# Performance work log

Hardware: AMD Instinct MI355X
Metric: run time of the kernel (lower is better)

The kernel has to match this reference:

```python
import jax, jax.numpy as jnp
import numpy as np
from jax import lax

EPS = 1e-5


def binarize(x):
    return jnp.sign(x)


def conv3x3(x, w):
    # x: NCHW, w: OIHW, stride 1, padding 1 (SAME for k=3)
    return lax.conv_general_dilated(
        x, w, window_strides=(1, 1), padding=((1, 1), (1, 1)),
        dimension_numbers=("NCHW", "OIHW", "NCHW"))


def prelu(x, a):
    # a broadcastable per-channel slope
    return jnp.where(x >= 0, x, a * x)


def bn(x, gamma, beta, axes):
    mean = jnp.mean(x, axis=axes, keepdims=True)
    var = jnp.var(x, axis=axes, keepdims=True)
    shp = [1] * x.ndim
    shp[1] = x.shape[1]
    g = gamma.reshape(shp)
    b = beta.reshape(shp)
    return (x - mean) * lax.rsqrt(var + EPS) * g + b


def setup_inputs() -> dict:
    key = jax.random.key(0)
    ks = jax.random.split(key, 8)
    B = 256
    C = [1, 64, 128]
    FC_IN = 28 * 28 * C[-1]  # 100352
    F1, F2 = 1024, 10
    inp = {
        "x": jax.random.normal(ks[0], (B, C[0], 28, 28), jnp.float32),
        "cw0": jax.random.normal(ks[1], (C[1], C[0], 3, 3), jnp.float32) * 0.1,
        "cp0": jnp.full((C[1],), 0.25, jnp.float32),
        "cg0": jnp.ones((C[1],), jnp.float32),
        "cb0": jnp.zeros((C[1],), jnp.float32),
        "cw1": jax.random.normal(ks[2], (C[2], C[1], 3, 3), jnp.float32) * 0.1,
        "cp1": jnp.full((C[2],), 0.25, jnp.float32),
        "cg1": jnp.ones((C[2],), jnp.float32),
        "cb1": jnp.zeros((C[2],), jnp.float32),
        "fw0": jax.random.normal(ks[3], (F1, FC_IN), jnp.float32) * 0.02,
        "fp0": jnp.full((F1,), 0.25, jnp.float32),
        "fg0": jnp.ones((F1,), jnp.float32),
        "fb0": jnp.zeros((F1,), jnp.float32),
        "fw1": jax.random.normal(ks[4], (F2, F1), jnp.float32) * 0.05,
        "fp1": jnp.full((F2,), 0.25, jnp.float32),
        "fg1": jnp.ones((F2,), jnp.float32),
        "fb1": jnp.zeros((F2,), jnp.float32),
        "scale": jnp.ones((1,), jnp.float32),
    }
    return inp


def reference(x, cw0, cp0, cg0, cb0, cw1, cp1, cg1, cb1,
              fw0, fp0, fg0, fb0, fw1, fp1, fg1, fb1, scale):
    # conv block 0
    h = binarize(x)
    h = conv3x3(h, jnp.sign(cw0))
    h = prelu(h, cp0[None, :, None, None])
    h = bn(h, cg0, cb0, axes=(0, 2, 3))
    # conv block 1
    h = binarize(h)
    h = conv3x3(h, jnp.sign(cw1))
    h = prelu(h, cp1[None, :, None, None])
    h = bn(h, cg1, cb1, axes=(0, 2, 3))
    # flatten
    h = h.reshape(-1, 28 * 28 * cw1.shape[0])
    # fc block 0
    h = binarize(h)
    h = h @ jnp.sign(fw0).T
    h = prelu(h, fp0[None, :])
    h = bn(h, fg0, fb0, axes=(0,))
    # fc block 1
    h = binarize(h)
    h = h @ jnp.sign(fw1).T
    h = prelu(h, fp1[None, :])
    h = bn(h, fg1, fb1, axes=(0,))
    # scale layer
    return h * scale
```

## Files before the change

### kernel.cpp

```cpp
#include <hip/hip_runtime.h>
#include <stdint.h>


static constexpr int BATCH = 256;
static constexpr int K0    = 100352;
static constexpr int KW    = 1568;
static constexpr int N1    = 1024;
static constexpr int KS2   = 49;
static constexpr int JW2   = 32;
static constexpr int SUB2  = 8;
static constexpr int NS2   = 4;
static constexpr unsigned ZCAP = 65536;

__device__ __forceinline__ float fsign(float v){
    return (v > 0.f) ? 1.f : ((v < 0.f) ? -1.f : 0.f);
}

__global__ __launch_bounds__(256) void k_pack_w1(const float* __restrict__ cw1,
        uint64_t* __restrict__ wn1, uint64_t* __restrict__ wnz1,
        int* __restrict__ zero_region)
{
    if (blockIdx.x == 0) {
        for (int i = threadIdx.x; i < 512; i += 256) zero_region[i] = 0;
    }
    int idx = blockIdx.x*4 + (threadIdx.x >> 6);
    int lane = threadIdx.x & 63;
    int oc = idx / 9, t = idx % 9;
    float w = cw1[oc*576 + lane*9 + t];
    uint64_t n = __ballot(w < 0.f);
    uint64_t z = __ballot(w != 0.f);
    if (lane == 0) { wn1[idx] = n; wnz1[idx] = z; }
}

__global__ __launch_bounds__(256) void k_conv0(const float* __restrict__ x,
        const float* __restrict__ cw0, const float* __restrict__ cp0,
        int8_t* __restrict__ h0s, double* __restrict__ S0, double* __restrict__ Q0)
{
    __shared__ float img[30][30];
    __shared__ float redS[4][64];
    __shared__ float redQ[4][64];
    int b = blockIdx.x;
    int tid = threadIdx.x;
    for (int i = tid; i < 900; i += 256) ((float*)img)[i] = 0.f;
    __syncthreads();
    for (int i = tid; i < 784; i += 256) {
        float v = x[b*784 + i];
        img[1 + i/28][1 + i%28] = fsign(v);
    }
    __syncthreads();
    int lane = tid & 63, wv = tid >> 6;
    float wsg[9];
    #pragma unroll
    for (int t = 0; t < 9; t++) wsg[t] = fsign(cw0[lane*9 + t]);
    float a = cp0[lane];
    float accS = 0.f, accQ = 0.f;
    for (int i = 0; i < 196; i++) {
        int p = wv*196 + i;
        int y = p / 28, xx = p % 28;
        float s = 0.f;
        #pragma unroll
        for (int dy = 0; dy < 3; dy++)
            #pragma unroll
            for (int dx = 0; dx < 3; dx++)
                s += img[y+dy][xx+dx] * wsg[dy*3+dx];
        h0s[(size_t)(b*784 + p)*64 + lane] = (int8_t)(int)s;
        float v = (s >= 0.f) ? s : a*s;
        accS += v; accQ += v*v;
    }
    redS[wv][lane] = accS; redQ[wv][lane] = accQ;
    __syncthreads();
    if (tid < 64) {
        double s = (double)redS[0][tid] + redS[1][tid] + redS[2][tid] + redS[3][tid];
        double q = (double)redQ[0][tid] + redQ[1][tid] + redQ[2][tid] + redQ[3][tid];
        atomicAdd(&S0[tid], s);
        atomicAdd(&Q0[tid], q);
    }
}

__global__ __launch_bounds__(256) void k_pack_h0(const int8_t* __restrict__ h0s,
        const double* __restrict__ S0, const double* __restrict__ Q0,
        const float* __restrict__ cg0, const float* __restrict__ cb0,
        const float* __restrict__ cp0, uint64_t* __restrict__ hp)
{
    __shared__ unsigned l[64];
    int tid = threadIdx.x;
    if (tid < 64) {
        double mean = S0[tid] * (1.0/200704.0);
        double var  = Q0[tid] * (1.0/200704.0) - mean*mean;
        if (var < 0.0) var = 0.0;
        double A = (double)cg0[tid] / sqrt(var + 1e-5);
        double B = (double)cb0[tid] - mean*A;
        float a = cp0[tid];
        unsigned m = 0;
        for (int s = -9; s <= 9; ++s) {
            float v = (s >= 0) ? (float)s : a*(float)s;
            if (fma((double)v, A, B) < 0.0) m |= 1u << (s + 9);
        }
        l[tid] = m;
    }
    __syncthreads();
    int pixel = blockIdx.x*256 + tid;
    const int4* p4 = (const int4*)(h0s + (size_t)pixel*64);
    int4 va = p4[0], vb = p4[1], vc = p4[2], vd = p4[3];
    int wa[16] = {va.x,va.y,va.z,va.w, vb.x,vb.y,vb.z,vb.w,
                  vc.x,vc.y,vc.z,vc.w, vd.x,vd.y,vd.z,vd.w};
    unsigned lo = 0, hi = 0;
    #pragma unroll
    for (int wi = 0; wi < 16; ++wi) {
        unsigned w = (unsigned)wa[wi];
        #pragma unroll
        for (int c2 = 0; c2 < 4; ++c2) {
            int ch = wi*4 + c2;
            int s = (int)(signed char)(w >> (8*c2));
            unsigned bit = (l[ch] >> (s + 9)) & 1u;
            if (ch < 32) lo |= bit << ch; else hi |= bit << (ch - 32);
        }
    }
    hp[pixel] = ((uint64_t)hi << 32) | lo;
}

__global__ __launch_bounds__(256) void k_conv1(const uint64_t* __restrict__ hp,
        const uint64_t* __restrict__ wn1, const uint64_t* __restrict__ wnz1,
        const float* __restrict__ cp1, int16_t* __restrict__ h1s,
        double* __restrict__ pS1, double* __restrict__ pQ1)
{
    __shared__ float lS[4][8];
    __shared__ float lQ[4][8];
    int bid = blockIdx.x;
    int ocg = bid & 15;
    int ptg = (bid >> 4) & 3;
    int b   = bid >> 6;
    int wv = threadIdx.x >> 6, lane = threadIdx.x & 63;
    int pt = ptg*4 + wv;
    bool active = (pt < 13);
    int p = active ? (pt*64 + lane) : 0;
    bool pvalid = active && (p < 784);
    int y = p / 28, xx = p % 28;
    uint64_t nb[9]; unsigned vmask = 0;
    #pragma unroll
    for (int dy = 0; dy < 3; dy++)
        #pragma unroll
        for (int dx = 0; dx < 3; dx++) {
            int t = dy*3+dx;
            int yy = y + dy - 1, xv = xx + dx - 1;
            bool ok = (yy >= 0 && yy < 28 && xv >= 0 && xv < 28);
            nb[t] = hp[b*784 + (ok ? (yy*28+xv) : 0)];
            if (ok) vmask |= 1u << t;
        }
    #pragma unroll
    for (int o = 0; o < 8; o++) {
        int oc = ocg*8 + o;
        int base = oc*9;
        int acc = 0;
        #pragma unroll
        for (int t = 0; t < 9; t++) {
            uint64_t wn = wn1[base+t], wz = wnz1[base+t];
            if (vmask & (1u<<t))
                acc += (int)__popcll(wz) - 2*(int)__popcll((nb[t] ^ wn) & wz);
        }
        if (pvalid) h1s[((size_t)b*128 + oc)*784 + p] = (int16_t)acc;
        float pr = cp1[oc];
        float v = pvalid ? ((acc >= 0) ? (float)acc : pr*(float)acc) : 0.f;
        float s = v, q = v*v;
        #pragma unroll
        for (int off = 32; off; off >>= 1) {
            s += __shfl_xor(s, off);
            q += __shfl_xor(q, off);
        }
        if (lane == 0) { lS[wv][o] = s; lQ[wv][o] = q; }
    }
    __syncthreads();
    if (threadIdx.x < 16) {
        int o = threadIdx.x & 7;
        bool isQ = threadIdx.x >= 8;
        double v4 = isQ ? ((double)lQ[0][o] + lQ[1][o] + lQ[2][o] + lQ[3][o])
                        : ((double)lS[0][o] + lS[1][o] + lS[2][o] + lS[3][o]);
        double* dst = isQ ? pQ1 : pS1;
        dst[(size_t)(ocg*8 + o)*1024 + (b*4 + ptg)] = v4;
    }
}

__global__ __launch_bounds__(256) void k_bnfin1(const double* __restrict__ pS,
        const double* __restrict__ pQ, const float* __restrict__ g,
        const float* __restrict__ bb, double* __restrict__ AB)
{
    int oc = blockIdx.x;
    int tid = threadIdx.x;
    double s = 0.0, q = 0.0;
    #pragma unroll
    for (int i = 0; i < 4; ++i) {
        s += pS[(size_t)oc*1024 + tid + 256*i];
        q += pQ[(size_t)oc*1024 + tid + 256*i];
    }
    __shared__ double rs[256], rq[256];
    rs[tid] = s; rq[tid] = q;
    __syncthreads();
    for (int off = 128; off; off >>= 1) {
        if (tid < off) { rs[tid] += rs[tid+off]; rq[tid] += rq[tid+off]; }
        __syncthreads();
    }
    if (tid == 0) {
        double mean = rs[0] * (1.0/200704.0);
        double var  = rq[0] * (1.0/200704.0) - mean*mean;
        if (var < 0.0) var = 0.0;
        double A = (double)g[oc] / sqrt(var + 1e-5);
        AB[oc] = A; AB[128 + oc] = (double)bb[oc] - mean*A;
    }
}

__global__ __launch_bounds__(256) void k_pack_a0(const int16_t* __restrict__ h1s,
        const float* __restrict__ cp1, const double* __restrict__ AB,
        uint64_t* __restrict__ ap_t)
{
    int blk = blockIdx.x;
    int b  = blk / 98;
    int qg = blk % 98;
    int wv = threadIdx.x >> 6, lane = threadIdx.x & 63;
    int q  = qg*4 + wv;
    int k0 = q*256 + lane*4;
    short4 sv = *(const short4*)(h1s + (size_t)b*K0 + k0);
    int oc = k0 / 784;
    double A = AB[oc], B = AB[128 + oc];
    float a = cp1[oc];
    int ss[4] = {sv.x, sv.y, sv.z, sv.w};
    uint64_t words[4];
    #pragma unroll
    for (int c = 0; c < 4; ++c) {
        float s = (float)ss[c];
        float v = (s >= 0.f) ? s : a*s;
        double t = fma((double)v, A, B);
        words[c] = __ballot(t < 0.0);
    }
    if (lane == 0) {
        #pragma unroll
        for (int c = 0; c < 4; ++c)
            ap_t[(size_t)(4*q + c)*256 + b] = words[c];
    }
}

__global__ __launch_bounds__(256) void k_fc0g(const float* __restrict__ fw0,
        const uint64_t* __restrict__ ap_t, int16_t* __restrict__ pcpart,
        unsigned* __restrict__ zcnt, uint64_t* __restrict__ zlist)
{
    __shared__ uint64_t wT[32][33];
    __shared__ uint64_t apL[SUB2][256];
    int ks = blockIdx.x % KS2;
    int nt = blockIdx.x / KS2;
    int tid = threadIdx.x;
    int wv = tid >> 6, lane = tid & 63;
    int n0 = nt*32, j0 = ks*JW2;
    {
        const float* wsrc = fw0 + (size_t)(n0 + wv*8)*K0 + (size_t)(ks*8)*256 + lane*4;
        for (int r8 = 0; r8 < 8; ++r8) {
            const float* rowp = wsrc + (size_t)r8*K0;
            int row = wv*8 + r8;
            #pragma unroll
            for (int qq = 0; qq < 8; ++qq) {
                float4 w = *(const float4*)(rowp + qq*256);
                uint64_t g0 = __ballot(w.x < 0.f);
                uint64_t g1 = __ballot(w.y < 0.f);
                uint64_t g2 = __ballot(w.z < 0.f);
                uint64_t g3 = __ballot(w.w < 0.f);
                uint64_t z0 = __ballot(w.x == 0.f);
                uint64_t z1 = __ballot(w.y == 0.f);
                uint64_t z2 = __ballot(w.z == 0.f);
                uint64_t z3 = __ballot(w.w == 0.f);
                if (lane == 0) {
                    wT[row][qq*4+0] = g0;
                    wT[row][qq*4+1] = g1;
                    wT[row][qq*4+2] = g2;
                    wT[row][qq*4+3] = g3;
                    uint64_t zz[4] = {z0, z1, z2, z3};
                    #pragma unroll
                    for (int c = 0; c < 4; ++c) if (zz[c]) {
                        unsigned id = atomicAdd(zcnt, 1u);
                        if (id < ZCAP) {
                            unsigned j = (unsigned)((ks*8 + qq)*4 + c);
                            zlist[2*id]   = ((uint64_t)(unsigned)(n0+row) << 32) | j;
                            zlist[2*id+1] = zz[c];
                        }
                    }
                }
            }
        }
    }
    int bq = tid & 31;
    int nq = tid >> 5;
    int pc[8][4];
    #pragma unroll
    for (int i = 0; i < 8; i++)
        #pragma unroll
        for (int k = 0; k < 4; k++) pc[i][k] = 0;
    for (int c = 0; c < NS2; c++) {
        #pragma unroll
        for (int r = 0; r < SUB2; r++)
            apL[r][tid] = ap_t[(size_t)(j0 + c*SUB2 + r)*256 + tid];
        __syncthreads();
        #pragma unroll
        for (int jj = 0; jj < SUB2; jj++) {
            uint64_t aw[8], ww[4];
            #pragma unroll
            for (int i = 0; i < 8; i++) aw[i] = apL[jj][bq + 32*i];
            #pragma unroll
            for (int k = 0; k < 4; k++) ww[k] = wT[nq + 8*k][c*8 + jj];
            #pragma unroll
            for (int i = 0; i < 8; i++)
                #pragma unroll
                for (int k = 0; k < 4; k++)
                    pc[i][k] += (int)__popcll(aw[i] ^ ww[k]);
        }
        __syncthreads();
    }
    #pragma unroll
    for (int k = 0; k < 4; k++) {
        int n = n0 + nq + 8*k;
        #pragma unroll
        for (int i = 0; i < 8; i++)
            pcpart[((size_t)ks*N1 + n)*BATCH + (bq + 32*i)] = (int16_t)pc[i][k];
    }
}

__global__ __launch_bounds__(256) void k_fc0ep(const int16_t* __restrict__ pcpart,
        const unsigned* __restrict__ zcnt, const uint64_t* __restrict__ zlist,
        const uint64_t* __restrict__ ap_t, const float* __restrict__ fp0,
        const float* __restrict__ fg0, const float* __restrict__ fb0,
        float* __restrict__ af)
{
    int n = blockIdx.x, b = threadIdx.x;
    int pc = 0;
    #pragma unroll
    for (int ks = 0; ks < KS2; ks++) pc += (int)pcpart[((size_t)ks*N1 + n)*BATCH + b];
    int s = K0 - 2*pc;
    unsigned cnt = *zcnt; if (cnt > ZCAP) cnt = ZCAP;
    for (unsigned e = 0; e < cnt; ++e) {
        uint64_t key = zlist[2*e];
        if ((int)(key >> 32) == n) {
            uint64_t zm = zlist[2*e+1];
            uint64_t a = ap_t[(size_t)(key & 0xffffffffu)*256 + b];
            s += 2*(int)__popcll(a & zm) - (int)__popcll(zm);
        }
    }
    float a = fp0[n];
    float v = (s >= 0) ? (float)s : a*(float)s;
    __shared__ double rs[256], rq[256];
    rs[b] = v; rq[b] = (double)v*(double)v;
    __syncthreads();
    for (int off=128; off>0; off>>=1){
        if (b<off){ rs[b]+=rs[b+off]; rq[b]+=rq[b+off]; }
        __syncthreads();
    }
    __shared__ double AB[2];
    if (b == 0) {
        double mean = rs[0] / 256.0;
        double var = rq[0] / 256.0 - mean*mean;
        if (var < 0.0) var = 0.0;
        double A = (double)fg0[n] / sqrt(var + 1e-5);
        AB[0] = A; AB[1] = (double)fb0[n] - mean*A;
    }
    __syncthreads();
    double t = fma((double)v, AB[0], AB[1]);
    af[(size_t)n*256 + b] = (t > 0.0) ? 1.f : ((t < 0.0) ? -1.f : 0.f);
}

__global__ __launch_bounds__(256) void k_fc1a(const float* __restrict__ af,
        const float* __restrict__ fw1, float* __restrict__ part9)
{
    __shared__ float swL[10][32];
    int ks = blockIdx.x, b = threadIdx.x;
    for (int i = b; i < 320; i += 256) {
        int j = i / 32, kk = i % 32;
        swL[j][kk] = fsign(fw1[j*1024 + ks*32 + kk]);
    }
    __syncthreads();
    float acc[10];
    #pragma unroll
    for (int j=0;j<10;j++) acc[j]=0.f;
    for (int kk = 0; kk < 32; kk++) {
        float a = af[(size_t)(ks*32+kk)*256 + b];
        #pragma unroll
        for (int j=0;j<10;j++) acc[j] += a * swL[j][kk];
    }
    #pragma unroll
    for (int j=0;j<10;j++) part9[((size_t)ks*256 + b)*10 + j] = acc[j];
}

__global__ __launch_bounds__(256) void k_fc1b(const float* __restrict__ part9,
        const float* __restrict__ fp1, const float* __restrict__ fg1,
        const float* __restrict__ fb1, const float* __restrict__ scale,
        float* __restrict__ out)
{
    int b = threadIdx.x;
    float v[10];
    #pragma unroll
    for (int j=0;j<10;j++) v[j]=0.f;
    for (int ks=0; ks<32; ks++)
        #pragma unroll
        for (int j=0;j<10;j++) v[j] += part9[((size_t)ks*256+b)*10 + j];
    #pragma unroll
    for (int j=0;j<10;j++){
        float a = fp1[j];
        v[j] = (v[j] >= 0.f) ? v[j] : a*v[j];
    }
    __shared__ double sv[256];
    __shared__ double AB[2][10];
    for (int j=0;j<10;j++){
        sv[b] = (double)v[j];
        __syncthreads();
        for (int off=128;off>0;off>>=1){ if(b<off) sv[b]+=sv[b+off]; __syncthreads(); }
        double mean = sv[0]/256.0;
        __syncthreads();
        double d = (double)v[j]-mean;
        sv[b] = d*d;
        __syncthreads();
        for (int off=128;off>0;off>>=1){ if(b<off) sv[b]+=sv[b+off]; __syncthreads(); }
        if (b==0){
            double var = sv[0]/256.0;
            double A = (double)fg1[j]/sqrt(var+1e-5);
            AB[0][j]=A; AB[1][j]=(double)fb1[j] - mean*A;
        }
        __syncthreads();
    }
    float sc = scale[0];
    #pragma unroll
    for (int j=0;j<10;j++)
        out[b*10+j] = (float)fma((double)v[j], AB[0][j], AB[1][j]) * sc;
}

extern "C" void kernel_launch(void* const* d_in, const int* in_sizes, int n_in,
                              void* d_out, int out_size, void* d_ws, size_t ws_size,
                              hipStream_t stream)
{
    const float* x    = (const float*)d_in[0];
    const float* cw0  = (const float*)d_in[1];
    const float* cp0  = (const float*)d_in[2];
    const float* cg0  = (const float*)d_in[3];
    const float* cb0  = (const float*)d_in[4];
    const float* cw1  = (const float*)d_in[5];
    const float* cp1  = (const float*)d_in[6];
    const float* cg1  = (const float*)d_in[7];
    const float* cb1  = (const float*)d_in[8];
    const float* fw0  = (const float*)d_in[9];
    const float* fp0  = (const float*)d_in[10];
    const float* fg0  = (const float*)d_in[11];
    const float* fb0  = (const float*)d_in[12];
    const float* fw1  = (const float*)d_in[13];
    const float* fp1  = (const float*)d_in[14];
    const float* fg1  = (const float*)d_in[15];
    const float* fb1  = (const float*)d_in[16];
    const float* scale= (const float*)d_in[17];

    char* ws = (char*)d_ws;
    size_t off = 0;
    auto alloc = [&](size_t bytes)->char* {
        char* r = ws + off; off = (off + bytes + 255) & ~(size_t)255; return r; };

    double*   S0    = (double*)alloc(64*8);
    double*   Q0    = (double*)alloc(64*8);
    unsigned* zcnt  = (unsigned*)alloc(256);
    double*   A1B1  = (double*)alloc(256*8);
    double*   pS1   = (double*)alloc((size_t)128*1024*8);
    double*   pQ1   = (double*)alloc((size_t)128*1024*8);
    int8_t*   h0s   = (int8_t*)alloc((size_t)256*784*64);
    uint64_t* hp    = (uint64_t*)alloc((size_t)256*784*8);
    int16_t*  h1s   = (int16_t*)alloc((size_t)256*128*784*2);
    uint64_t* ap_t  = (uint64_t*)alloc((size_t)KW*256*8);
    uint64_t* wn1   = (uint64_t*)alloc(1152*8);
    uint64_t* wnz1  = (uint64_t*)alloc(1152*8);
    int16_t*  pcpart= (int16_t*)alloc((size_t)KS2*N1*BATCH*2);
    float*    af    = (float*)alloc((size_t)1024*256*4);
    float*    part9 = (float*)alloc((size_t)32*256*10*4);
    uint64_t* zlist = (uint64_t*)alloc((size_t)ZCAP*16);
    (void)ws_size; (void)in_sizes; (void)n_in; (void)out_size;

    k_pack_w1<<<288,     256, 0, stream>>>(cw1, wn1, wnz1, (int*)d_ws);
    k_conv0  <<<256,     256, 0, stream>>>(x, cw0, cp0, h0s, S0, Q0);
    k_pack_h0<<<784,     256, 0, stream>>>(h0s, S0, Q0, cg0, cb0, cp0, hp);
    k_conv1  <<<16384,   256, 0, stream>>>(hp, wn1, wnz1, cp1, h1s, pS1, pQ1);
    k_bnfin1 <<<128,     256, 0, stream>>>(pS1, pQ1, cg1, cb1, A1B1);
    k_pack_a0<<<256*98,  256, 0, stream>>>(h1s, cp1, A1B1, ap_t);
    k_fc0g   <<<KS2*32,  256, 0, stream>>>(fw0, ap_t, pcpart, zcnt, zlist);
    k_fc0ep  <<<1024,    256, 0, stream>>>(pcpart, zcnt, zlist, ap_t, fp0, fg0, fb0, af);
    k_fc1a   <<<32,      256, 0, stream>>>(af, fw1, part9);
    k_fc1b   <<<1,       256, 0, stream>>>(part9, fp1, fg1, fb1, scale, (float*)d_out);
}
```

Baseline: 350.6 us.

## Loop conv1 over pixel groups per block, precompute weight popcounts, fuse fc1 kernels

```diff
diff --git a/kernel.cpp b/kernel.cpp
--- a/kernel.cpp
+++ b/kernel.cpp
@@ -18,10 +18,10 @@
 
 __global__ __launch_bounds__(256) void k_pack_w1(const float* __restrict__ cw1,
         uint64_t* __restrict__ wn1, uint64_t* __restrict__ wnz1,
-        int* __restrict__ zero_region)
+        int* __restrict__ wzc, int* __restrict__ zero_region)
 {
     if (blockIdx.x == 0) {
-        for (int i = threadIdx.x; i < 512; i += 256) zero_region[i] = 0;
+        for (int i = threadIdx.x; i < 320; i += 256) zero_region[i] = 0;
     }
     int idx = blockIdx.x*4 + (threadIdx.x >> 6);
     int lane = threadIdx.x & 63;
@@ -29,7 +29,7 @@
     float w = cw1[oc*576 + lane*9 + t];
     uint64_t n = __ballot(w < 0.f);
     uint64_t z = __ballot(w != 0.f);
-    if (lane == 0) { wn1[idx] = n; wnz1[idx] = z; }
+    if (lane == 0) { wn1[idx] = n; wnz1[idx] = z; wzc[idx] = (int)__popcll(z); }
 }
 
 __global__ __launch_bounds__(256) void k_conv0(const float* __restrict__ x,
@@ -121,47 +121,58 @@
 
 __global__ __launch_bounds__(256) void k_conv1(const uint64_t* __restrict__ hp,
         const uint64_t* __restrict__ wn1, const uint64_t* __restrict__ wnz1,
-        const float* __restrict__ cp1, int16_t* __restrict__ h1s,
-        double* __restrict__ pS1, double* __restrict__ pQ1)
+        const int* __restrict__ wzc, const float* __restrict__ cp1,
+        int16_t* __restrict__ h1s, double* __restrict__ pS1, double* __restrict__ pQ1)
 {
     __shared__ float lS[4][8];
     __shared__ float lQ[4][8];
     int bid = blockIdx.x;
     int ocg = bid & 15;
-    int ptg = (bid >> 4) & 3;
-    int b   = bid >> 6;
+    int b   = bid >> 4;
     int wv = threadIdx.x >> 6, lane = threadIdx.x & 63;
-    int pt = ptg*4 + wv;
-    bool active = (pt < 13);
-    int p = active ? (pt*64 + lane) : 0;
-    bool pvalid = active && (p < 784);
-    int y = p / 28, xx = p % 28;
-    uint64_t nb[9]; unsigned vmask = 0;
-    #pragma unroll
-    for (int dy = 0; dy < 3; dy++)
-        #pragma unroll
-        for (int dx = 0; dx < 3; dx++) {
-            int t = dy*3+dx;
-            int yy = y + dy - 1, xv = xx + dx - 1;
-            bool ok = (yy >= 0 && yy < 28 && xv >= 0 && xv < 28);
-            nb[t] = hp[b*784 + (ok ? (yy*28+xv) : 0)];
-            if (ok) vmask |= 1u << t;
-        }
+    float pr[8];
+    #pragma unroll
+    for (int o = 0; o < 8; o++) pr[o] = cp1[ocg*8 + o];
+    float sA[8], qA[8];
+    #pragma unroll
+    for (int o = 0; o < 8; o++) { sA[o] = 0.f; qA[o] = 0.f; }
+
+    for (int ptg = 0; ptg < 4; ++ptg) {
+        int pt = ptg*4 + wv;
+        bool active = (pt < 13);
+        int p = active ? (pt*64 + lane) : 0;
+        bool pvalid = active && (p < 784);
+        int y = p / 28, xx = p % 28;
+        uint64_t nb[9]; unsigned vmask = 0;
+        #pragma unroll
+        for (int dy = 0; dy < 3; dy++)
+            #pragma unroll
+            for (int dx = 0; dx < 3; dx++) {
+                int t = dy*3+dx;
+                int yy = y + dy - 1, xv = xx + dx - 1;
+                bool ok = (yy >= 0 && yy < 28 && xv >= 0 && xv < 28);
+                nb[t] = hp[b*784 + (ok ? (yy*28+xv) : 0)];
+                if (ok) vmask |= 1u << t;
+            }
+        #pragma unroll
+        for (int o = 0; o < 8; o++) {
+            int base = (ocg*8 + o)*9;
+            int acc = 0;
+            #pragma unroll
+            for (int t = 0; t < 9; t++) {
+                uint64_t wn = wn1[base+t], wz = wnz1[base+t];
+                int wc = wzc[base+t];
+                if (vmask & (1u<<t))
+                    acc += wc - 2*(int)__popcll((nb[t] ^ wn) & wz);
+            }
+            if (pvalid) h1s[((size_t)b*128 + ocg*8 + o)*784 + p] = (int16_t)acc;
+            float v = pvalid ? ((acc >= 0) ? (float)acc : pr[o]*(float)acc) : 0.f;
+            sA[o] += v; qA[o] += v*v;
+        }
+    }
     #pragma unroll
     for (int o = 0; o < 8; o++) {
-        int oc = ocg*8 + o;
-        int base = oc*9;
-        int acc = 0;
-        #pragma unroll
-        for (int t = 0; t < 9; t++) {
-            uint64_t wn = wn1[base+t], wz = wnz1[base+t];
-            if (vmask & (1u<<t))
-                acc += (int)__popcll(wz) - 2*(int)__popcll((nb[t] ^ wn) & wz);
-        }
-        if (pvalid) h1s[((size_t)b*128 + oc)*784 + p] = (int16_t)acc;
-        float pr = cp1[oc];
-        float v = pvalid ? ((acc >= 0) ? (float)acc : pr*(float)acc) : 0.f;
-        float s = v, q = v*v;
+        float s = sA[o], q = qA[o];
         #pragma unroll
         for (int off = 32; off; off >>= 1) {
             s += __shfl_xor(s, off);
@@ -176,7 +187,7 @@
         double v4 = isQ ? ((double)lQ[0][o] + lQ[1][o] + lQ[2][o] + lQ[3][o])
                         : ((double)lS[0][o] + lS[1][o] + lS[2][o] + lS[3][o]);
         double* dst = isQ ? pQ1 : pS1;
-        dst[(size_t)(ocg*8 + o)*1024 + (b*4 + ptg)] = v4;
+        dst[(size_t)(ocg*8 + o)*256 + b] = v4;
     }
 }
 
@@ -186,14 +197,9 @@
 {
     int oc = blockIdx.x;
     int tid = threadIdx.x;
-    double s = 0.0, q = 0.0;
-    #pragma unroll
-    for (int i = 0; i < 4; ++i) {
-        s += pS[(size_t)oc*1024 + tid + 256*i];
-        q += pQ[(size_t)oc*1024 + tid + 256*i];
-    }
     __shared__ double rs[256], rq[256];
-    rs[tid] = s; rq[tid] = q;
+    rs[tid] = pS[(size_t)oc*256 + tid];
+    rq[tid] = pQ[(size_t)oc*256 + tid];
     __syncthreads();
     for (int off = 128; off; off >>= 1) {
         if (tid < off) { rs[tid] += rs[tid+off]; rq[tid] += rq[tid+off]; }
@@ -270,14 +276,16 @@
                     wT[row][qq*4+1] = g1;
                     wT[row][qq*4+2] = g2;
                     wT[row][qq*4+3] = g3;
-                    uint64_t zz[4] = {z0, z1, z2, z3};
-                    #pragma unroll
-                    for (int c = 0; c < 4; ++c) if (zz[c]) {
-                        unsigned id = atomicAdd(zcnt, 1u);
-                        if (id < ZCAP) {
-                            unsigned j = (unsigned)((ks*8 + qq)*4 + c);
-                            zlist[2*id]   = ((uint64_t)(unsigned)(n0+row) << 32) | j;
-                            zlist[2*id+1] = zz[c];
+                    if (z0 | z1 | z2 | z3) {
+                        uint64_t zz[4] = {z0, z1, z2, z3};
+                        #pragma unroll
+                        for (int c = 0; c < 4; ++c) if (zz[c]) {
+                            unsigned id = atomicAdd(zcnt, 1u);
+                            if (id < ZCAP) {
+                                unsigned j = (unsigned)((ks*8 + qq)*4 + c);
+                                zlist[2*id]   = ((uint64_t)(unsigned)(n0+row) << 32) | j;
+                                zlist[2*id+1] = zz[c];
+                            }
                         }
                     }
                 }
@@ -362,68 +370,41 @@
     af[(size_t)n*256 + b] = (t > 0.0) ? 1.f : ((t < 0.0) ? -1.f : 0.f);
 }
 
-__global__ __launch_bounds__(256) void k_fc1a(const float* __restrict__ af,
-        const float* __restrict__ fw1, float* __restrict__ part9)
-{
-    __shared__ float swL[10][32];
-    int ks = blockIdx.x, b = threadIdx.x;
-    for (int i = b; i < 320; i += 256) {
-        int j = i / 32, kk = i % 32;
-        swL[j][kk] = fsign(fw1[j*1024 + ks*32 + kk]);
-    }
-    __syncthreads();
-    float acc[10];
-    #pragma unroll
-    for (int j=0;j<10;j++) acc[j]=0.f;
-    for (int kk = 0; kk < 32; kk++) {
-        float a = af[(size_t)(ks*32+kk)*256 + b];
-        #pragma unroll
-        for (int j=0;j<10;j++) acc[j] += a * swL[j][kk];
-    }
-    #pragma unroll
-    for (int j=0;j<10;j++) part9[((size_t)ks*256 + b)*10 + j] = acc[j];
-}
-
-__global__ __launch_bounds__(256) void k_fc1b(const float* __restrict__ part9,
-        const float* __restrict__ fp1, const float* __restrict__ fg1,
-        const float* __restrict__ fb1, const float* __restrict__ scale,
-        float* __restrict__ out)
-{
-    int b = threadIdx.x;
-    float v[10];
-    #pragma unroll
-    for (int j=0;j<10;j++) v[j]=0.f;
-    for (int ks=0; ks<32; ks++)
-        #pragma unroll
-        for (int j=0;j<10;j++) v[j] += part9[((size_t)ks*256+b)*10 + j];
-    #pragma unroll
-    for (int j=0;j<10;j++){
-        float a = fp1[j];
-        v[j] = (v[j] >= 0.f) ? v[j] : a*v[j];
-    }
+__global__ __launch_bounds__(256) void k_fc1(const float* __restrict__ af,
+        const float* __restrict__ fw1, const float* __restrict__ fp1,
+        const float* __restrict__ fg1, const float* __restrict__ fb1,
+        const float* __restrict__ scale, float* __restrict__ out)
+{
     __shared__ double sv[256];
-    __shared__ double AB[2][10];
-    for (int j=0;j<10;j++){
-        sv[b] = (double)v[j];
-        __syncthreads();
-        for (int off=128;off>0;off>>=1){ if(b<off) sv[b]+=sv[b+off]; __syncthreads(); }
-        double mean = sv[0]/256.0;
-        __syncthreads();
-        double d = (double)v[j]-mean;
-        sv[b] = d*d;
-        __syncthreads();
-        for (int off=128;off>0;off>>=1){ if(b<off) sv[b]+=sv[b+off]; __syncthreads(); }
-        if (b==0){
-            double var = sv[0]/256.0;
-            double A = (double)fg1[j]/sqrt(var+1e-5);
-            AB[0][j]=A; AB[1][j]=(double)fb1[j] - mean*A;
-        }
-        __syncthreads();
-    }
-    float sc = scale[0];
-    #pragma unroll
-    for (int j=0;j<10;j++)
-        out[b*10+j] = (float)fma((double)v[j], AB[0][j], AB[1][j]) * sc;
+    __shared__ double ABj[2];
+    int j = blockIdx.x, b = threadIdx.x;
+    float acc = 0.f;
+    for (int k = 0; k < 1024; ++k)
+        acc += af[(size_t)k*256 + b] * fsign(fw1[j*1024 + k]);
+    float a = fp1[j];
+    float v = (acc >= 0.f) ? acc : a*acc;
+    sv[b] = (double)v;
+    __syncthreads();
+    for (int off = 128; off > 0; off >>= 1) {
+        if (b < off) sv[b] += sv[b+off];
+        __syncthreads();
+    }
+    double mean = sv[0] / 256.0;
+    __syncthreads();
+    double d = (double)v - mean;
+    sv[b] = d*d;
+    __syncthreads();
+    for (int off = 128; off > 0; off >>= 1) {
+        if (b < off) sv[b] += sv[b+off];
+        __syncthreads();
+    }
+    if (b == 0) {
+        double var = sv[0] / 256.0;
+        double A = (double)fg1[j] / sqrt(var + 1e-5);
+        ABj[0] = A; ABj[1] = (double)fb1[j] - mean*A;
+    }
+    __syncthreads();
+    out[b*10 + j] = (float)fma((double)v, ABj[0], ABj[1]) * scale[0];
 }
 
 extern "C" void kernel_launch(void* const* d_in, const int* in_sizes, int n_in,
@@ -458,8 +439,9 @@
     double*   Q0    = (double*)alloc(64*8);
     unsigned* zcnt  = (unsigned*)alloc(256);
     double*   A1B1  = (double*)alloc(256*8);
-    double*   pS1   = (double*)alloc((size_t)128*1024*8);
-    double*   pQ1   = (double*)alloc((size_t)128*1024*8);
+    double*   pS1   = (double*)alloc((size_t)128*256*8);
+    double*   pQ1   = (double*)alloc((size_t)128*256*8);
+    int*      wzc   = (int*)alloc(1152*4);
     int8_t*   h0s   = (int8_t*)alloc((size_t)256*784*64);
     uint64_t* hp    = (uint64_t*)alloc((size_t)256*784*8);
     int16_t*  h1s   = (int16_t*)alloc((size_t)256*128*784*2);
@@ -468,18 +450,16 @@
     uint64_t* wnz1  = (uint64_t*)alloc(1152*8);
     int16_t*  pcpart= (int16_t*)alloc((size_t)KS2*N1*BATCH*2);
     float*    af    = (float*)alloc((size_t)1024*256*4);
-    float*    part9 = (float*)alloc((size_t)32*256*10*4);
     uint64_t* zlist = (uint64_t*)alloc((size_t)ZCAP*16);
     (void)ws_size; (void)in_sizes; (void)n_in; (void)out_size;
 
-    k_pack_w1<<<288,     256, 0, stream>>>(cw1, wn1, wnz1, (int*)d_ws);
-    k_conv0  <<<256,     256, 0, stream>>>(x, cw0, cp0, h0s, S0, Q0);
-    k_pack_h0<<<784,     256, 0, stream>>>(h0s, S0, Q0, cg0, cb0, cp0, hp);
-    k_conv1  <<<16384,   256, 0, stream>>>(hp, wn1, wnz1, cp1, h1s, pS1, pQ1);
-    k_bnfin1 <<<128,     256, 0, stream>>>(pS1, pQ1, cg1, cb1, A1B1);
-    k_pack_a0<<<256*98,  256, 0, stream>>>(h1s, cp1, A1B1, ap_t);
-    k_fc0g   <<<KS2*32,  256, 0, stream>>>(fw0, ap_t, pcpart, zcnt, zlist);
-    k_fc0ep  <<<1024,    256, 0, stream>>>(pcpart, zcnt, zlist, ap_t, fp0, fg0, fb0, af);
-    k_fc1a   <<<32,      256, 0, stream>>>(af, fw1, part9);
-    k_fc1b   <<<1,       256, 0, stream>>>(part9, fp1, fg1, fb1, scale, (float*)d_out);
-}
+    k_pack_w1<<<288,   256, 0, stream>>>(cw1, wn1, wnz1, wzc, (int*)d_ws);
+    k_conv0  <<<256,   256, 0, stream>>>(x, cw0, cp0, h0s, S0, Q0);
+    k_pack_h0<<<784,   256, 0, stream>>>(h0s, S0, Q0, cg0, cb0, cp0, hp);
+    k_conv1  <<<4096,  256, 0, stream>>>(hp, wn1, wnz1, wzc, cp1, h1s, pS1, pQ1);
+    k_bnfin1 <<<128,   256, 0, stream>>>(pS1, pQ1, cg1, cb1, A1B1);
+    k_pack_a0<<<25088, 256, 0, stream>>>(h1s, cp1, A1B1, ap_t);
+    k_fc0g   <<<KS2*32,256, 0, stream>>>(fw0, ap_t, pcpart, zcnt, zlist);
+    k_fc0ep  <<<1024,  256, 0, stream>>>(pcpart, zcnt, zlist, ap_t, fp0, fg0, fb0, af);
+    k_fc1    <<<10,    256, 0, stream>>>(af, fw1, fp1, fg1, fb1, scale, (float*)d_out);
+}
```

Result: slower. 456.5 us (+30.2%).
